# Performance work log

Measured on AMD Instinct MI355X. Metric: run time of the kernel, lower is better.

Reference implementation:

```python
import jax, jax.numpy as jnp
import numpy as np

D = 128
N_ROUNDS = 8


def _lin(k, fan_in, fan_out):
    return jax.random.normal(k, (fan_in, fan_out), jnp.float32) * (1.0 / np.sqrt(fan_in)).astype(np.float32)


def setup_inputs() -> dict:
    key = jax.random.key(0)
    ks = jax.random.split(key, 10)
    n_vars, n_clauses, n_edges = 65536, 262144, 1048576
    n_lits = 2 * n_vars
    clause_index = jax.random.randint(ks[0], (n_edges,), 0, n_clauses)
    literal_index = jax.random.randint(ks[1], (n_edges,), 0, n_lits)
    return {
        "n_vars": n_vars,
        "n_clauses": n_clauses,
        "clause_index": clause_index,
        "literal_index": literal_index,
        "L_init_scale": jnp.float32(1.0 / np.sqrt(D)),
        "C_init_scale": jnp.float32(1.0 / np.sqrt(D)),
        "LC_scale": jnp.float32(0.1),
        "CL_scale": jnp.float32(0.1),
        # C update MLP: [C, LC_msgs] (2d) -> d -> d
        "C_W1": _lin(ks[2], 2 * D, D), "C_b1": jnp.zeros((D,), jnp.float32),
        "C_W2": _lin(ks[3], D, D),     "C_b2": jnp.zeros((D,), jnp.float32),
        # L update MLP: [L, CL_msgs, flip(L)] (3d) -> d -> d
        "L_W1": _lin(ks[4], 3 * D, D), "L_b1": jnp.zeros((D,), jnp.float32),
        "L_W2": _lin(ks[5], D, D),     "L_b2": jnp.zeros((D,), jnp.float32),
        # V score MLP: [L_pos, L_neg] (2d) -> d -> 1
        "V_W1": _lin(ks[6], 2 * D, D), "V_b1": jnp.zeros((D,), jnp.float32),
        "V_W2": _lin(ks[7], D, 1),     "V_b2": jnp.zeros((1,), jnp.float32),
    }


def _mlp(x, W1, b1, W2, b2):
    # 2-layer MLP, relu on hidden layer only
    return jnp.maximum(x @ W1 + b1, 0.0) @ W2 + b2


def reference(n_vars, n_clauses, clause_index, literal_index,
              L_init_scale, C_init_scale, LC_scale, CL_scale,
              C_W1, C_b1, C_W2, C_b2,
              L_W1, L_b1, L_W2, L_b2,
              V_W1, V_b1, V_W2, V_b2):
    d = C_W2.shape[1]
    n_lits = 2 * n_vars
    L0 = jnp.ones((n_lits, d), jnp.float32) * L_init_scale
    C0 = jnp.ones((n_clauses, d), jnp.float32) * C_init_scale

    def flip(Lm):
        # swap positive/negative literal embeddings per variable
        pl, ul = jnp.split(Lm.reshape(n_vars, 2 * d), 2, axis=1)
        return jnp.concatenate([ul, pl], axis=1).reshape(n_lits, d)

    def step(carry, _):
        L, C = carry
        # literal -> clause messages (gather + segment sum)
        LC_msgs = jax.ops.segment_sum(L[literal_index], clause_index,
                                      num_segments=n_clauses) * LC_scale
        C_new = _mlp(jnp.concatenate([C, LC_msgs], axis=-1),
                     C_W1, C_b1, C_W2, C_b2) + C  # res_layers
        # clause -> literal messages
        CL_msgs = jax.ops.segment_sum(C_new[clause_index], literal_index,
                                      num_segments=n_lits) * CL_scale
        L_new = _mlp(jnp.concatenate([L, CL_msgs, flip(L)], axis=-1),
                     L_W1, L_b1, L_W2, L_b2) + L  # res_layers
        return (L_new, C_new), None

    (L, C), _ = jax.lax.scan(step, (L0, C0), None, length=N_ROUNDS)
    V = L.reshape(n_vars, 2 * d)
    V_scores = _mlp(V, V_W1, V_b1, V_W2, V_b2)
    return V_scores[:, 0]  # pi_core_var_logits
```

## Files before the change

kernel.cpp:

```cpp
#include <hip/hip_runtime.h>
#include <cstddef>

#define D_    128
#define NV_   65536
#define NL_   131072
#define NC_   262144
#define NE_   1048576
#define NROUNDS_ 8

typedef __attribute__((ext_vector_type(4)))  short short4v;
typedef __attribute__((ext_vector_type(8)))  short short8v;
typedef __attribute__((ext_vector_type(16))) float f32x16;

__device__ __forceinline__ float4 f4_load(const float* p) { return *(const float4*)p; }
__device__ __forceinline__ void   f4_store(float* p, float4 v) { *(float4*)p = v; }
__device__ __forceinline__ float4 f4_zero() { return make_float4(0.f, 0.f, 0.f, 0.f); }
__device__ __forceinline__ float4 f4_add(float4 a, float4 b) {
    a.x += b.x; a.y += b.y; a.z += b.z; a.w += b.w; return a;
}
__device__ __forceinline__ float4 f4_scale(float4 a, float s) {
    a.x *= s; a.y *= s; a.z *= s; a.w *= s; return a;
}

__device__ __forceinline__ void micro_fma(const float4 a[4], const float4 w[4], float4 acc[4]) {
#pragma unroll
    for (int i = 0; i < 4; i++) {
        float4 av = a[i];
        acc[i].x += av.x * w[0].x; acc[i].x += av.y * w[1].x; acc[i].x += av.z * w[2].x; acc[i].x += av.w * w[3].x;
        acc[i].y += av.x * w[0].y; acc[i].y += av.y * w[1].y; acc[i].y += av.z * w[2].y; acc[i].y += av.w * w[3].y;
        acc[i].z += av.x * w[0].z; acc[i].z += av.y * w[1].z; acc[i].z += av.z * w[2].z; acc[i].z += av.w * w[3].z;
        acc[i].w += av.x * w[0].w; acc[i].w += av.y * w[1].w; acc[i].w += av.z * w[2].w; acc[i].w += av.w * w[3].w;
    }
}

template<int KD, bool FLIP>
__device__ __forceinline__ void layer1_to_H(float* Xs, float* Wcs,
        const float* __restrict__ W1, const float* __restrict__ b1, int t)
{
    const int tr = t >> 5, tc = t & 31;
    float4 acc[4];
    acc[0] = acc[1] = acc[2] = acc[3] = f4_zero();
#pragma unroll 1
    for (int kc = 0; kc < KD; kc += 32) {
        __syncthreads();
#pragma unroll
        for (int i = t; i < 1024; i += 256)
            ((float4*)Wcs)[i] = ((const float4*)W1)[kc * 32 + i];
        __syncthreads();
        const bool fl = FLIP && (kc >= 256);
        const int ab = fl ? (kc - 256) : kc;
#pragma unroll
        for (int k = 0; k < 32; k += 4) {
            float4 a[4], w[4];
#pragma unroll
            for (int i = 0; i < 4; i++) {
                int r = 4 * tr + i;
                if (fl) r ^= 1;
                a[i] = f4_load(Xs + r * 256 + ab + k);
            }
#pragma unroll
            for (int kk = 0; kk < 4; kk++)
                w[kk] = f4_load(Wcs + (k + kk) * 128 + 4 * tc);
            micro_fma(a, w, acc);
        }
    }
    float4 bv = f4_load(b1 + 4 * tc);
    __syncthreads();
#pragma unroll
    for (int i = 0; i < 4; i++) {
        float4 h;
        h.x = fmaxf(acc[i].x + bv.x, 0.f);
        h.y = fmaxf(acc[i].y + bv.y, 0.f);
        h.z = fmaxf(acc[i].z + bv.z, 0.f);
        h.w = fmaxf(acc[i].w + bv.w, 0.f);
        f4_store(Xs + (4 * tr + i) * 256 + 128 + 4 * tc, h);
    }
}

__device__ __forceinline__ unsigned short f2bf(float x) {
    unsigned u = __float_as_uint(x);
    u += 0x7fffu + ((u >> 16) & 1u);
    return (unsigned short)(u >> 16);
}
__device__ __forceinline__ float bf2f(unsigned short h) {
    return __uint_as_float(((unsigned)h) << 16);
}
__device__ __forceinline__ void split_bf(float x, unsigned short& h, unsigned short& l) {
    h = f2bf(x);
    l = f2bf(x - bf2f(h));
}
__device__ __forceinline__ void cvt4(const float4& a, short4v& h, short4v& l) {
    unsigned short h0,h1,h2,h3,l0,l1,l2,l3;
    split_bf(a.x,h0,l0); split_bf(a.y,h1,l1); split_bf(a.z,h2,l2); split_bf(a.w,h3,l3);
    h = (short4v){(short)h0,(short)h1,(short)h2,(short)h3};
    l = (short4v){(short)l0,(short)l1,(short)l2,(short)l3};
}
__device__ __forceinline__ void cvt8(const float4& a, const float4& b, short8v& h, short8v& l) {
    unsigned short h0,h1,h2,h3,h4,h5,h6,h7,l0,l1,l2,l3,l4,l5,l6,l7;
    split_bf(a.x,h0,l0); split_bf(a.y,h1,l1); split_bf(a.z,h2,l2); split_bf(a.w,h3,l3);
    split_bf(b.x,h4,l4); split_bf(b.y,h5,l5); split_bf(b.z,h6,l6); split_bf(b.w,h7,l7);
    h = (short8v){(short)h0,(short)h1,(short)h2,(short)h3,(short)h4,(short)h5,(short)h6,(short)h7};
    l = (short8v){(short)l0,(short)l1,(short)l2,(short)l3,(short)l4,(short)l5,(short)l6,(short)l7};
}

__device__ __forceinline__ int aswz(int r, int k) { return (r * 512 + k * 2) ^ ((r & 7) << 4); }
__device__ __forceinline__ int hswz(int r, int k) { return (r * 256 + k * 2) ^ ((r & 7) << 4); }

__global__ void pack_weights(const float* __restrict__ W, short* __restrict__ out, int K)
{
    int o = blockIdx.x * 256 + threadIdx.x;
    if (o >= 2 * K * 128) return;
    int i = o & 7;
    int g = o >> 3;
    int n  = g & 127;
    int kk = (g >> 7) & 3;
    int p  = (g >> 9) & 1;
    int c  = g >> 10;
    int k  = c * 32 + kk * 8 + i;
    float x = W[k * 128 + n];
    unsigned short h = f2bf(x);
    unsigned short v = p ? f2bf(x - bf2f(h)) : h;
    out[o] = (short)v;
}

__global__ void fill_kernel(float* __restrict__ L, float* __restrict__ C,
                            const float* __restrict__ lsp, const float* __restrict__ csp)
{
    const float ls = *lsp, cs = *csp;
    const size_t stride = (size_t)gridDim.x * blockDim.x;
    size_t i0 = (size_t)blockIdx.x * blockDim.x + threadIdx.x;
    const size_t nL = (size_t)NL_ * D_ / 4, nC = (size_t)NC_ * D_ / 4;
    float4 lv = make_float4(ls, ls, ls, ls), cv = make_float4(cs, cs, cs, cs);
    for (size_t i = i0; i < nL; i += stride) ((float4*)L)[i] = lv;
    for (size_t i = i0; i < nC; i += stride) ((float4*)C)[i] = cv;
}

__global__ void count_kernel(const int* __restrict__ ci, const int* __restrict__ li,
                             int* __restrict__ ccnt, int* __restrict__ lcnt)
{
    int e = blockIdx.x * 256 + threadIdx.x;
    if (e < NE_) {
        atomicAdd(&ccnt[ci[e]], 1);
        atomicAdd(&lcnt[li[e]], 1);
    }
}

__global__ void scan_block(const int* __restrict__ in, int* __restrict__ out,
                           int* __restrict__ bsum)
{
    __shared__ int sh[256];
    const int t = threadIdx.x;
    const int base = blockIdx.x * 1024 + t * 4;
    int v0 = in[base], v1 = in[base + 1], v2 = in[base + 2], v3 = in[base + 3];
    int s = v0 + v1 + v2 + v3;
    sh[t] = s;
    __syncthreads();
    for (int off = 1; off < 256; off <<= 1) {
        int y = (t >= off) ? sh[t - off] : 0;
        __syncthreads();
        sh[t] += y;
        __syncthreads();
    }
    int excl = sh[t] - s;
    out[base + 0] = excl;
    out[base + 1] = excl + v0;
    out[base + 2] = excl + v0 + v1;
    out[base + 3] = excl + v0 + v1 + v2;
    if (t == 255) bsum[blockIdx.x] = sh[255];
}

__global__ void scan_top(int* __restrict__ bs, int n)
{
    __shared__ int sh[256];
    const int t = threadIdx.x;
    int v = (t < n) ? bs[t] : 0;
    sh[t] = v;
    __syncthreads();
    for (int off = 1; off < 256; off <<= 1) {
        int y = (t >= off) ? sh[t - off] : 0;
        __syncthreads();
        sh[t] += y;
        __syncthreads();
    }
    if (t < n) bs[t] = sh[t] - v;
}

__global__ void scan_add(int* __restrict__ offs, const int* __restrict__ bs,
                         int* __restrict__ cur, int n, int total)
{
    int i = blockIdx.x * 256 + threadIdx.x;
    if (i < n) {
        int v = offs[i] + bs[i >> 10];
        offs[i] = v;
        cur[i] = v;
    }
    if (i == 0) offs[n] = total;
}

__global__ void fill_csr(const int* __restrict__ ci, const int* __restrict__ li,
                         int* __restrict__ ccur, int* __restrict__ lcur,
                         int* __restrict__ cedges, int* __restrict__ ledges)
{
    int e = blockIdx.x * 256 + threadIdx.x;
    if (e < NE_) {
        int c = ci[e], l = li[e];
        int p = atomicAdd(&ccur[c], 1); cedges[p] = l;
        int q = atomicAdd(&lcur[l], 1); ledges[q] = c;
    }
}

template<int K1, bool FLIP>
__global__ __launch_bounds__(256, 4) void update_mfma(
        float* __restrict__ Mat, const float* __restrict__ Src,
        const int* __restrict__ offs, const int* __restrict__ eidx,
        const short* __restrict__ Wp1, const float* __restrict__ b1,
        const short* __restrict__ Wp2, const float* __restrict__ b2,
        const float* __restrict__ scale_p)
{
    __shared__ __align__(16) unsigned char SM[49152];
    unsigned char* sm = SM;
    const int t = threadIdx.x;
    const int base = blockIdx.x * 32;
    const int lane = t & 63, w = t >> 6;
    const int rA = lane & 31;
    const int kg = lane >> 5;
    const int nB = w * 32 + rA;

#pragma unroll
    for (int i = t; i < 1024; i += 256) {
        int r = i >> 5, q = i & 31;
        float4 v = ((const float4*)Mat)[(size_t)base * 32 + i];
        short4v hv, lv;
        cvt4(v, hv, lv);
        *(short4v*)(sm + aswz(r, 4 * q)) = hv;
        *(short4v*)(sm + 16384 + aswz(r, 4 * q)) = lv;
    }
    {
        const float sc = *scale_p;
        const int r = t >> 3, s = t & 7;
        const int row = base + r;
        const int e0 = offs[row], e1 = offs[row + 1];
        float4 a0 = f4_zero(), a1 = f4_zero(), a2 = f4_zero(), a3 = f4_zero();
        int e = e0;
        for (; e + 1 < e1; e += 2) {
            const float* P = Src + (size_t)eidx[e] * 128 + s * 16;
            const float* Q = Src + (size_t)eidx[e + 1] * 128 + s * 16;
            float4 p0 = f4_load(P), p1 = f4_load(P + 4), p2 = f4_load(P + 8), p3 = f4_load(P + 12);
            float4 q0 = f4_load(Q), q1 = f4_load(Q + 4), q2 = f4_load(Q + 8), q3 = f4_load(Q + 12);
            a0 = f4_add(a0, p0); a1 = f4_add(a1, p1); a2 = f4_add(a2, p2); a3 = f4_add(a3, p3);
            a0 = f4_add(a0, q0); a1 = f4_add(a1, q1); a2 = f4_add(a2, q2); a3 = f4_add(a3, q3);
        }
        if (e < e1) {
            const float* P = Src + (size_t)eidx[e] * 128 + s * 16;
            a0 = f4_add(a0, f4_load(P));
            a1 = f4_add(a1, f4_load(P + 4));
            a2 = f4_add(a2, f4_load(P + 8));
            a3 = f4_add(a3, f4_load(P + 12));
        }
        a0 = f4_scale(a0, sc); a1 = f4_scale(a1, sc);
        a2 = f4_scale(a2, sc); a3 = f4_scale(a3, sc);
        short8v h0, l0, h1, l1;
        cvt8(a0, a1, h0, l0);
        cvt8(a2, a3, h1, l1);
        const int k0 = 128 + 16 * s;
        *(short8v*)(sm + aswz(r, k0))             = h0;
        *(short8v*)(sm + aswz(r, k0 + 8))         = h1;
        *(short8v*)(sm + 16384 + aswz(r, k0))     = l0;
        *(short8v*)(sm + 16384 + aswz(r, k0 + 8)) = l1;
    }
    __syncthreads();

    f32x16 c0, c1;
#pragma unroll
    for (int i = 0; i < 16; ++i) { c0[i] = 0.f; c1[i] = 0.f; }

#pragma unroll 2
    for (int st = 0; st < K1 / 16; ++st) {
        const int c = st >> 1, kk = (st & 1) * 2 + kg;
        int ka = st * 16 + kg * 8;
        int ar = rA;
        if (FLIP && st >= 16) { ar = rA ^ 1; ka -= 256; }
        short8v ah = *(const short8v*)(sm + aswz(ar, ka));
        short8v al = *(const short8v*)(sm + 16384 + aswz(ar, ka));
        const short* W = Wp1 + c * 8192;
        short8v bh = *(const short8v*)(W + ((size_t)(kk * 128 + nB)) * 8);
        short8v bl = *(const short8v*)(W + ((size_t)((4 + kk) * 128 + nB)) * 8);
        c0 = __builtin_amdgcn_mfma_f32_32x32x16_bf16(ah, bh, c0, 0, 0, 0);
        c1 = __builtin_amdgcn_mfma_f32_32x32x16_bf16(ah, bl, c1, 0, 0, 0);
        c1 = __builtin_amdgcn_mfma_f32_32x32x16_bf16(al, bh, c1, 0, 0, 0);
    }

    {
        const float b = b1[nB];
#pragma unroll
        for (int i = 0; i < 16; ++i) {
            int row = (i & 3) + 8 * (i >> 2) + 4 * kg;
            float h = fmaxf(c0[i] + c1[i] + b, 0.f);
            unsigned short hh, hl;
            split_bf(h, hh, hl);
            *(short*)(sm + 32768 + hswz(row, nB)) = (short)hh;
            *(short*)(sm + 40960 + hswz(row, nB)) = (short)hl;
        }
    }
    __syncthreads();

#pragma unroll
    for (int i = 0; i < 16; ++i) { c0[i] = 0.f; c1[i] = 0.f; }
#pragma unroll 2
    for (int st = 0; st < 8; ++st) {
        const int c = st >> 1, kk = (st & 1) * 2 + kg;
        const int ka = st * 16 + kg * 8;
        short8v ah = *(const short8v*)(sm + 32768 + hswz(rA, ka));
        short8v al = *(const short8v*)(sm + 40960 + hswz(rA, ka));
        const short* W = Wp2 + c * 8192;
        short8v bh = *(const short8v*)(W + ((size_t)(kk * 128 + nB)) * 8);
        short8v bl = *(const short8v*)(W + ((size_t)((4 + kk) * 128 + nB)) * 8);
        c0 = __builtin_amdgcn_mfma_f32_32x32x16_bf16(ah, bh, c0, 0, 0, 0);
        c1 = __builtin_amdgcn_mfma_f32_32x32x16_bf16(ah, bl, c1, 0, 0, 0);
        c1 = __builtin_amdgcn_mfma_f32_32x32x16_bf16(al, bh, c1, 0, 0, 0);
    }

    {
        const float b = b2[nB];
#pragma unroll
        for (int i = 0; i < 16; ++i) {
            int row = (i & 3) + 8 * (i >> 2) + 4 * kg;
            size_t gi = (size_t)(base + row) * 128 + nB;
            Mat[gi] = c0[i] + c1[i] + b + Mat[gi];
        }
    }
}

__global__ __launch_bounds__(256) void v_score(
        float* __restrict__ out, const float* __restrict__ Lmat,
        const float* __restrict__ W1, const float* __restrict__ b1,
        const float* __restrict__ W2, const float* __restrict__ b2)
{
    __shared__ float Xs[32 * 256];
    __shared__ float Wcs[32 * 128];
    const int t = threadIdx.x;
    const int base = blockIdx.x * 32;

#pragma unroll
    for (int i = t; i < 2048; i += 256)
        ((float4*)Xs)[i] = ((const float4*)Lmat)[(size_t)base * 64 + i];

    layer1_to_H<256, false>(Xs, Wcs, W1, b1, t);
    __syncthreads();
    if (t < 32) ((float4*)Wcs)[t] = ((const float4*)W2)[t];
    __syncthreads();

    const int r = t >> 3, s = t & 7;
    float sum = 0.f;
#pragma unroll
    for (int j = 0; j < 16; j++)
        sum += Xs[r * 256 + 128 + s * 16 + j] * Wcs[s * 16 + j];
    sum += __shfl_xor(sum, 1);
    sum += __shfl_xor(sum, 2);
    sum += __shfl_xor(sum, 4);
    if (s == 0) out[base + r] = sum + b2[0];
}

extern "C" void kernel_launch(void* const* d_in, const int* in_sizes, int n_in,
                              void* d_out, int out_size, void* d_ws, size_t ws_size,
                              hipStream_t stream)
{
    const int*   ci   = (const int*)d_in[2];
    const int*   li   = (const int*)d_in[3];
    const float* Lsc  = (const float*)d_in[4];
    const float* Csc  = (const float*)d_in[5];
    const float* LCsc = (const float*)d_in[6];
    const float* CLsc = (const float*)d_in[7];
    const float* C_W1 = (const float*)d_in[8];
    const float* C_b1 = (const float*)d_in[9];
    const float* C_W2 = (const float*)d_in[10];
    const float* C_b2 = (const float*)d_in[11];
    const float* L_W1 = (const float*)d_in[12];
    const float* L_b1 = (const float*)d_in[13];
    const float* L_W2 = (const float*)d_in[14];
    const float* L_b2 = (const float*)d_in[15];
    const float* V_W1 = (const float*)d_in[16];
    const float* V_b1 = (const float*)d_in[17];
    const float* V_W2 = (const float*)d_in[18];
    const float* V_b2 = (const float*)d_in[19];
    float* out = (float*)d_out;

    char* w = (char*)d_ws;
    float* Cmat  = (float*)w; w += (size_t)NC_ * D_ * 4;
    float* Lmat  = (float*)w; w += (size_t)NL_ * D_ * 4;
    int* coffs   = (int*)w;   w += (size_t)(NC_ + 1) * 4;
    int* ccur    = (int*)w;   w += (size_t)NC_ * 4;
    int* cedges  = (int*)w;   w += (size_t)NE_ * 4;
    int* loffs   = (int*)w;   w += (size_t)(NL_ + 1) * 4;
    int* lcur    = (int*)w;   w += (size_t)NL_ * 4;
    int* ledges  = (int*)w;   w += (size_t)NE_ * 4;
    int* bsumC   = (int*)w;   w += 256 * 4;
    int* bsumL   = (int*)w;   w += 256 * 4;
    short* WpC1  = (short*)w; w += (size_t)2 * 256 * 128 * 2;
    short* WpC2  = (short*)w; w += (size_t)2 * 128 * 128 * 2;
    short* WpL1  = (short*)w; w += (size_t)2 * 384 * 128 * 2;
    short* WpL2  = (short*)w; w += (size_t)2 * 128 * 128 * 2;

    hipMemsetAsync(ccur, 0, (size_t)NC_ * 4, stream);
    hipMemsetAsync(lcur, 0, (size_t)NL_ * 4, stream);

    pack_weights<<<(2 * 256 * 128) / 256, 256, 0, stream>>>(C_W1, WpC1, 256);
    pack_weights<<<(2 * 128 * 128) / 256, 256, 0, stream>>>(C_W2, WpC2, 128);
    pack_weights<<<(2 * 384 * 128) / 256, 256, 0, stream>>>(L_W1, WpL1, 384);
    pack_weights<<<(2 * 128 * 128) / 256, 256, 0, stream>>>(L_W2, WpL2, 128);

    fill_kernel<<<2048, 256, 0, stream>>>(Lmat, Cmat, Lsc, Csc);
    count_kernel<<<NE_ / 256, 256, 0, stream>>>(ci, li, ccur, lcur);

    scan_block<<<NC_ / 1024, 256, 0, stream>>>(ccur, coffs, bsumC);
    scan_top<<<1, 256, 0, stream>>>(bsumC, NC_ / 1024);
    scan_add<<<NC_ / 256, 256, 0, stream>>>(coffs, bsumC, ccur, NC_, NE_);

    scan_block<<<NL_ / 1024, 256, 0, stream>>>(lcur, loffs, bsumL);
    scan_top<<<1, 256, 0, stream>>>(bsumL, NL_ / 1024);
    scan_add<<<NL_ / 256, 256, 0, stream>>>(loffs, bsumL, lcur, NL_, NE_);

    fill_csr<<<NE_ / 256, 256, 0, stream>>>(ci, li, ccur, lcur, cedges, ledges);

    for (int r = 0; r < NROUNDS_; r++) {
        update_mfma<256, false><<<NC_ / 32, 256, 0, stream>>>(
            Cmat, Lmat, coffs, cedges, WpC1, C_b1, WpC2, C_b2, LCsc);
        update_mfma<384, true><<<NL_ / 32, 256, 0, stream>>>(
            Lmat, Cmat, loffs, ledges, WpL1, L_b1, WpL2, L_b2, CLsc);
    }
    v_score<<<NV_ / 32, 256, 0, stream>>>(out, Lmat, V_W1, V_b1, V_W2, V_b2);
}
```

Before: 3.178 ms.

## Reduce update kernel LDS by staging messages after self-part GEMM

Shared memory shrinks from 48KB to 32KB. The aggregated message tile is now held in registers while the self (and flipped) part of the first GEMM runs, then written into the same LDS region for the message part. This lets launch bounds rise to 5 blocks per CU to improve occupancy for the latency-bound gather. In exchange it adds an extra barrier and keeps more live registers across the first MFMA phase, which may spill at the tighter register budget.

```diff
diff --git a/kernel.cpp b/kernel.cpp
--- a/kernel.cpp
+++ b/kernel.cpp
@@ -103,8 +103,7 @@
     l = (short8v){(short)l0,(short)l1,(short)l2,(short)l3,(short)l4,(short)l5,(short)l6,(short)l7};
 }
 
-__device__ __forceinline__ int aswz(int r, int k) { return (r * 512 + k * 2) ^ ((r & 7) << 4); }
-__device__ __forceinline__ int hswz(int r, int k) { return (r * 256 + k * 2) ^ ((r & 7) << 4); }
+__device__ __forceinline__ int pswz(int r, int k) { return (r * 256 + k * 2) ^ ((r & 7) << 4); }
 
 __global__ void pack_weights(const float* __restrict__ W, short* __restrict__ out, int K)
 {
@@ -209,15 +208,15 @@
     }
 }
 
-template<int K1, bool FLIP>
-__global__ __launch_bounds__(256, 4) void update_mfma(
+template<bool FLIP>
+__global__ __launch_bounds__(256, 5) void update_mfma(
         float* __restrict__ Mat, const float* __restrict__ Src,
         const int* __restrict__ offs, const int* __restrict__ eidx,
         const short* __restrict__ Wp1, const float* __restrict__ b1,
         const short* __restrict__ Wp2, const float* __restrict__ b2,
         const float* __restrict__ scale_p)
 {
-    __shared__ __align__(16) unsigned char SM[49152];
+    __shared__ __align__(16) unsigned char SM[32768];
     unsigned char* sm = SM;
     const int t = threadIdx.x;
     const int base = blockIdx.x * 32;
@@ -232,26 +231,27 @@
         float4 v = ((const float4*)Mat)[(size_t)base * 32 + i];
         short4v hv, lv;
         cvt4(v, hv, lv);
-        *(short4v*)(sm + aswz(r, 4 * q)) = hv;
-        *(short4v*)(sm + 16384 + aswz(r, 4 * q)) = lv;
-    }
+        *(short4v*)(sm + pswz(r, 4 * q)) = hv;
+        *(short4v*)(sm + 8192 + pswz(r, 4 * q)) = lv;
+    }
+    short8v mh0, ml0, mh1, ml1;
+    const int gr = t >> 3, gs = t & 7;
     {
         const float sc = *scale_p;
-        const int r = t >> 3, s = t & 7;
-        const int row = base + r;
+        const int row = base + gr;
         const int e0 = offs[row], e1 = offs[row + 1];
         float4 a0 = f4_zero(), a1 = f4_zero(), a2 = f4_zero(), a3 = f4_zero();
         int e = e0;
         for (; e + 1 < e1; e += 2) {
-            const float* P = Src + (size_t)eidx[e] * 128 + s * 16;
-            const float* Q = Src + (size_t)eidx[e + 1] * 128 + s * 16;
+            const float* P = Src + (size_t)eidx[e] * 128 + gs * 16;
+            const float* Q = Src + (size_t)eidx[e + 1] * 128 + gs * 16;
             float4 p0 = f4_load(P), p1 = f4_load(P + 4), p2 = f4_load(P + 8), p3 = f4_load(P + 12);
             float4 q0 = f4_load(Q), q1 = f4_load(Q + 4), q2 = f4_load(Q + 8), q3 = f4_load(Q + 12);
             a0 = f4_add(a0, p0); a1 = f4_add(a1, p1); a2 = f4_add(a2, p2); a3 = f4_add(a3, p3);
             a0 = f4_add(a0, q0); a1 = f4_add(a1, q1); a2 = f4_add(a2, q2); a3 = f4_add(a3, q3);
         }
         if (e < e1) {
-            const float* P = Src + (size_t)eidx[e] * 128 + s * 16;
+            const float* P = Src + (size_t)eidx[e] * 128 + gs * 16;
             a0 = f4_add(a0, f4_load(P));
             a1 = f4_add(a1, f4_load(P + 4));
             a2 = f4_add(a2, f4_load(P + 8));
@@ -259,14 +259,8 @@
         }
         a0 = f4_scale(a0, sc); a1 = f4_scale(a1, sc);
         a2 = f4_scale(a2, sc); a3 = f4_scale(a3, sc);
-        short8v h0, l0, h1, l1;
-        cvt8(a0, a1, h0, l0);
-        cvt8(a2, a3, h1, l1);
-        const int k0 = 128 + 16 * s;
-        *(short8v*)(sm + aswz(r, k0))             = h0;
-        *(short8v*)(sm + aswz(r, k0 + 8))         = h1;
-        *(short8v*)(sm + 16384 + aswz(r, k0))     = l0;
-        *(short8v*)(sm + 16384 + aswz(r, k0 + 8)) = l1;
+        cvt8(a0, a1, mh0, ml0);
+        cvt8(a2, a3, mh1, ml1);
     }
     __syncthreads();
 
@@ -274,21 +268,40 @@
 #pragma unroll
     for (int i = 0; i < 16; ++i) { c0[i] = 0.f; c1[i] = 0.f; }
 
+#define MFMA_STEP(Wp, st, ka, ar, HB) do {                                          \
+        short8v ah = *(const short8v*)(sm + (HB) + pswz((ar), (ka)));               \
+        short8v al = *(const short8v*)(sm + (HB) + 8192 + pswz((ar), (ka)));        \
+        const short* Wc = (Wp) + ((st) >> 1) * 8192;                                \
+        const int kk = ((st) & 1) * 2 + kg;                                         \
+        short8v bh = *(const short8v*)(Wc + ((size_t)(kk * 128 + nB)) * 8);         \
+        short8v bl = *(const short8v*)(Wc + ((size_t)((4 + kk) * 128 + nB)) * 8);   \
+        c0 = __builtin_amdgcn_mfma_f32_32x32x16_bf16(ah, bh, c0, 0, 0, 0);          \
+        c1 = __builtin_amdgcn_mfma_f32_32x32x16_bf16(ah, bl, c1, 0, 0, 0);          \
+        c1 = __builtin_amdgcn_mfma_f32_32x32x16_bf16(al, bh, c1, 0, 0, 0);          \
+    } while (0)
+
 #pragma unroll 2
-    for (int st = 0; st < K1 / 16; ++st) {
-        const int c = st >> 1, kk = (st & 1) * 2 + kg;
-        int ka = st * 16 + kg * 8;
-        int ar = rA;
-        if (FLIP && st >= 16) { ar = rA ^ 1; ka -= 256; }
-        short8v ah = *(const short8v*)(sm + aswz(ar, ka));
-        short8v al = *(const short8v*)(sm + 16384 + aswz(ar, ka));
-        const short* W = Wp1 + c * 8192;
-        short8v bh = *(const short8v*)(W + ((size_t)(kk * 128 + nB)) * 8);
-        short8v bl = *(const short8v*)(W + ((size_t)((4 + kk) * 128 + nB)) * 8);
-        c0 = __builtin_amdgcn_mfma_f32_32x32x16_bf16(ah, bh, c0, 0, 0, 0);
-        c1 = __builtin_amdgcn_mfma_f32_32x32x16_bf16(ah, bl, c1, 0, 0, 0);
-        c1 = __builtin_amdgcn_mfma_f32_32x32x16_bf16(al, bh, c1, 0, 0, 0);
-    }
+    for (int st = 0; st < 8; ++st)
+        MFMA_STEP(Wp1, st, st * 16 + kg * 8, rA, 0);
+    if (FLIP) {
+#pragma unroll 2
+        for (int st = 16; st < 24; ++st)
+            MFMA_STEP(Wp1, st, (st - 16) * 16 + kg * 8, rA ^ 1, 0);
+    }
+    __syncthreads();
+
+    {
+        const int k0 = 16 * gs;
+        *(short8v*)(sm + pswz(gr, k0))            = mh0;
+        *(short8v*)(sm + pswz(gr, k0 + 8))        = mh1;
+        *(short8v*)(sm + 8192 + pswz(gr, k0))     = ml0;
+        *(short8v*)(sm + 8192 + pswz(gr, k0 + 8)) = ml1;
+    }
+    __syncthreads();
+
+#pragma unroll 2
+    for (int st = 8; st < 16; ++st)
+        MFMA_STEP(Wp1, st, (st - 8) * 16 + kg * 8, rA, 0);
 
     {
         const float b = b1[nB];
@@ -298,8 +311,8 @@
             float h = fmaxf(c0[i] + c1[i] + b, 0.f);
             unsigned short hh, hl;
             split_bf(h, hh, hl);
-            *(short*)(sm + 32768 + hswz(row, nB)) = (short)hh;
-            *(short*)(sm + 40960 + hswz(row, nB)) = (short)hl;
+            *(short*)(sm + 16384 + pswz(row, nB)) = (short)hh;
+            *(short*)(sm + 24576 + pswz(row, nB)) = (short)hl;
         }
     }
     __syncthreads();
@@ -307,18 +320,9 @@
 #pragma unroll
     for (int i = 0; i < 16; ++i) { c0[i] = 0.f; c1[i] = 0.f; }
 #pragma unroll 2
-    for (int st = 0; st < 8; ++st) {
-        const int c = st >> 1, kk = (st & 1) * 2 + kg;
-        const int ka = st * 16 + kg * 8;
-        short8v ah = *(const short8v*)(sm + 32768 + hswz(rA, ka));
-        short8v al = *(const short8v*)(sm + 40960 + hswz(rA, ka));
-        const short* W = Wp2 + c * 8192;
-        short8v bh = *(const short8v*)(W + ((size_t)(kk * 128 + nB)) * 8);
-        short8v bl = *(const short8v*)(W + ((size_t)((4 + kk) * 128 + nB)) * 8);
-        c0 = __builtin_amdgcn_mfma_f32_32x32x16_bf16(ah, bh, c0, 0, 0, 0);
-        c1 = __builtin_amdgcn_mfma_f32_32x32x16_bf16(ah, bl, c1, 0, 0, 0);
-        c1 = __builtin_amdgcn_mfma_f32_32x32x16_bf16(al, bh, c1, 0, 0, 0);
-    }
+    for (int st = 0; st < 8; ++st)
+        MFMA_STEP(Wp2, st, st * 16 + kg * 8, rA, 16384);
+#undef MFMA_STEP
 
     {
         const float b = b2[nB];
@@ -423,9 +427,9 @@
     fill_csr<<<NE_ / 256, 256, 0, stream>>>(ci, li, ccur, lcur, cedges, ledges);
 
     for (int r = 0; r < NROUNDS_; r++) {
-        update_mfma<256, false><<<NC_ / 32, 256, 0, stream>>>(
+        update_mfma<false><<<NC_ / 32, 256, 0, stream>>>(
             Cmat, Lmat, coffs, cedges, WpC1, C_b1, WpC2, C_b2, LCsc);
-        update_mfma<384, true><<<NL_ / 32, 256, 0, stream>>>(
+        update_mfma<true><<<NL_ / 32, 256, 0, stream>>>(
             Lmat, Cmat, loffs, ledges, WpL1, L_b1, WpL2, L_b2, CLsc);
     }
     v_score<<<NV_ / 32, 256, 0, stream>>>(out, Lmat, V_W1, V_b1, V_W2, V_b2);
```

New measurement: 3.026 ms. 1.05x faster.
